# Kernel tuning notes

Hardware: AMD Instinct MI355X
Metric: run time of the kernel (lower is better)

The kernel has to match this reference:

```python
import jax, jax.numpy as jnp
import numpy as np

# dims: batch, encoder frames, encoder dim, pred-net hidden, joint dim, vocab (blank = V)
B, T, ENC, H, J, V = 32, 64, 1024, 320, 320, 1024
BLANK = V
MAXSYM = 2            # max_symbols_per_step
S = T * MAXSYM        # upper bound on loop-labels iterations (<= MAXSYM steps per frame due to force-blank)


def setup_inputs() -> dict:
    key = jax.random.key(0)
    ks = jax.random.split(key, 10)
    s = 0.05
    return {
        "x": jax.random.normal(ks[0], (B, T, ENC), jnp.float32),
        "out_len": jax.random.randint(ks[1], (B,), T // 2, T + 1, dtype=jnp.int32),
        "W_enc": jax.random.normal(ks[2], (ENC, J), jnp.float32) * s,
        "b_enc": jnp.zeros((J,), jnp.float32),
        "Emb": jax.random.normal(ks[3], (V, H), jnp.float32) * s,
        "W_ih": jax.random.normal(ks[4], (H, 4 * H), jnp.float32) * s,
        "W_hh": jax.random.normal(ks[5], (H, 4 * H), jnp.float32) * s,
        "b_lstm": jnp.zeros((4 * H,), jnp.float32),
        "W_pred": jax.random.normal(ks[6], (H, J), jnp.float32) * s,
        "b_pred": jnp.zeros((J,), jnp.float32),
        "W_out": jax.random.normal(ks[7], (J, V + 1), jnp.float32) * s,
        "b_out": jnp.zeros((V + 1,), jnp.float32),
    }


def _lstm_step(emb, h, c, W_ih, W_hh, b):
    g = emb @ W_ih + h @ W_hh + b
    i, f, gg, o = jnp.split(g, 4, axis=-1)
    c2 = jax.nn.sigmoid(f) * c + jax.nn.sigmoid(i) * jnp.tanh(gg)
    h2 = jax.nn.sigmoid(o) * jnp.tanh(c2)
    return h2, c2


def reference(x, out_len, W_enc, b_enc, Emb, W_ih, W_hh, b_lstm, W_pred, b_pred, W_out, b_out):
    # project_encoder once (as in the torch module)
    x_proj = x @ W_enc + b_enc                      # [B, T, J]
    # SOS step: zero embedding, zero LSTM state (decoder.predict(None, None))
    z = jnp.zeros((B, H), x.dtype)
    h0, c0 = _lstm_step(z, z, z, W_ih, W_hh, b_lstm)
    dec0 = h0 @ W_pred + b_pred                     # project_prednet

    def step(carry, _):
        time, symbols, h, c, dec = carry
        enc_t = jnp.take_along_axis(x_proj, time[:, None, None].astype(jnp.int32), axis=1)[:, 0]  # [B, J]
        logits = jax.nn.relu(enc_t + dec) @ W_out + b_out  # joint_after_projection, [B, V+1]
        scores = logits.max(-1)
        labels = jnp.argmax(logits, -1)
        active = time < out_len
        emit = active & (labels != BLANK)
        # prediction-network step for elements that emitted a non-blank label
        emb = Emb[jnp.where(emit, labels, 0)]
        h2, c2 = _lstm_step(emb, h, c, W_ih, W_hh, b_lstm)
        dec2 = h2 @ W_pred + b_pred
        m = emit[:, None]
        h = jnp.where(m, h2, h)
        c = jnp.where(m, c2, c)
        dec = jnp.where(m, dec2, dec)
        sym2 = jnp.where(emit, symbols + 1, jnp.zeros_like(symbols))
        force = emit & (sym2 >= MAXSYM)             # force blank after max_symbols on one frame
        advance = (active & ~emit) | force          # blank (or forced blank) advances time
        time2 = time + advance.astype(time.dtype)
        sym2 = jnp.where(advance, jnp.zeros_like(sym2), sym2)
        out = (jnp.where(emit, labels, BLANK).astype(jnp.int32),
               jnp.where(active, scores, jnp.zeros_like(scores)),
               time.astype(jnp.int32),
               emit)
        return (time2, sym2, h, c, dec), out

    init = (jnp.zeros((B,), jnp.int32), jnp.zeros((B,), jnp.int32), h0, c0, dec0)
    _, (lab, sc, tm, em) = jax.lax.scan(step, init, None, length=S)
    lengths = em.astype(jnp.int32).sum(0)
    # lab/sc/tm: [S, B] alignment-style records (BLANK filler when nothing emitted);
    # lengths: number of emitted (non-blank) labels per utterance -> equals batched_hyps contents.
    return lab, sc, tm, lengths
```

## Files before the change

### kernel.cpp

```cpp
#include <hip/hip_runtime.h>
#include <math.h>

typedef unsigned long long ull;

constexpr int Bn = 32, Tn = 64, Hn = 320, Jn = 320, Vn = 1024, Sn = 128;
constexpr int G4n = 1280, VP1 = 1025, WO4S = 1028;

constexpr int OFF_XP  = 0;
constexpr int OFF_G   = OFF_XP + Bn*Tn*Jn;
constexpr int OFF_WO4 = OFF_G + Vn*G4n;
constexpr int OFF_WH4 = OFF_WO4 + 80*WO4S*4;
constexpr int OFF_WP4 = OFF_WH4 + 80*G4n*4;
constexpr int OFF_CB  = OFF_WP4 + 80*Jn*4;
constexpr int OFF_DEC = OFF_CB + 2*Bn*Hn;
constexpr int OFF_GB  = OFF_DEC + 2*Bn*Jn;
constexpr int OFF_KEY = OFF_GB + 2*Bn*G4n;
constexpr int OFF_REC = OFF_KEY + 2*Bn*40*2;

__device__ __forceinline__ float sigmf(float x) { return 1.0f / (1.0f + expf(-x)); }

__device__ __forceinline__ ull pack_key(float v, int idx) {
    unsigned u = __float_as_uint(v);
    u = (u & 0x80000000u) ? ~u : (u | 0x80000000u);
    return ((ull)u << 32) | (unsigned)(0x7FFFFFFF - idx);
}
__device__ __forceinline__ float key_val(ull k) {
    unsigned u = (unsigned)(k >> 32);
    return __uint_as_float((u & 0x80000000u) ? (u & 0x7FFFFFFFu) : ~u);
}
__device__ __forceinline__ int key_idx(ull k) { return 0x7FFFFFFF - (int)(k & 0xFFFFFFFFu); }

__global__ __launch_bounds__(256) void gemm_bias(const float* __restrict__ A,
                                                 const float* __restrict__ Bm,
                                                 const float* __restrict__ bias,
                                                 float* __restrict__ C,
                                                 int M, int N, int K) {
    __shared__ float As[16][65];
    __shared__ float Bs[16][65];
    const int tx = threadIdx.x & 15, ty = threadIdx.x >> 4;
    const int n0 = blockIdx.x * 64, m0 = blockIdx.y * 64;
    float acc[4][4] = {};
    for (int k0 = 0; k0 < K; k0 += 16) {
        for (int i = threadIdx.x; i < 1024; i += 256) {
            int mm = i >> 4, kk = i & 15;
            As[kk][mm] = A[(m0 + mm) * K + k0 + kk];
            int kk2 = i >> 6, nn = i & 63;
            Bs[kk2][nn] = Bm[(k0 + kk2) * N + n0 + nn];
        }
        __syncthreads();
#pragma unroll
        for (int kk = 0; kk < 16; ++kk) {
            float av[4], bv[4];
#pragma unroll
            for (int r = 0; r < 4; ++r) { av[r] = As[kk][ty * 4 + r]; bv[r] = Bs[kk][tx * 4 + r]; }
#pragma unroll
            for (int i2 = 0; i2 < 4; ++i2)
#pragma unroll
                for (int j2 = 0; j2 < 4; ++j2) acc[i2][j2] += av[i2] * bv[j2];
        }
        __syncthreads();
    }
#pragma unroll
    for (int i2 = 0; i2 < 4; ++i2)
#pragma unroll
        for (int j2 = 0; j2 < 4; ++j2)
            C[(m0 + ty * 4 + i2) * N + n0 + tx * 4 + j2] = acc[i2][j2] + bias[n0 + tx * 4 + j2];
}

__global__ __launch_bounds__(256) void repack_wout4(const float* __restrict__ W,
                                                    float* __restrict__ W4) {
    const int k4 = blockIdx.x;
    for (int c = threadIdx.x; c < VP1; c += 256) {
        float4 v;
        v.x = W[(k4 * 4 + 0) * VP1 + c];
        v.y = W[(k4 * 4 + 1) * VP1 + c];
        v.z = W[(k4 * 4 + 2) * VP1 + c];
        v.w = W[(k4 * 4 + 3) * VP1 + c];
        ((float4*)W4)[(size_t)k4 * WO4S + c] = v;
    }
}
__global__ __launch_bounds__(256) void repack_whh4(const float* __restrict__ W,
                                                   float* __restrict__ W4) {
    const int k4 = blockIdx.x;
    for (int c = threadIdx.x; c < G4n; c += 256) {
        float4 v;
        v.x = W[(k4 * 4 + 0) * G4n + c];
        v.y = W[(k4 * 4 + 1) * G4n + c];
        v.z = W[(k4 * 4 + 2) * G4n + c];
        v.w = W[(k4 * 4 + 3) * G4n + c];
        ((float4*)W4)[(size_t)k4 * G4n + c] = v;
    }
}
__global__ __launch_bounds__(256) void repack_wpred4(const float* __restrict__ W,
                                                     float* __restrict__ W4) {
    const int k4 = blockIdx.x;
    for (int c = threadIdx.x; c < Jn; c += 256) {
        float4 v;
        v.x = W[(k4 * 4 + 0) * Jn + c];
        v.y = W[(k4 * 4 + 1) * Jn + c];
        v.z = W[(k4 * 4 + 2) * Jn + c];
        v.w = W[(k4 * 4 + 3) * Jn + c];
        ((float4*)W4)[(size_t)k4 * Jn + c] = v;
    }
}

__global__ __launch_bounds__(256, 1) void rnnt_step(
    const float* __restrict__ xp, const float* __restrict__ Gm,
    const float* __restrict__ Wo4, const float* __restrict__ Wh4,
    const float* __restrict__ Wp4,
    const float* __restrict__ b_out, const float* __restrict__ b_lstm,
    const float* __restrict__ b_pred, const int* __restrict__ out_len,
    float* __restrict__ cb, float* __restrict__ db, float* __restrict__ gb,
    ull* __restrict__ keys, int* __restrict__ rec, float* __restrict__ out,
    int L) {
    __shared__ __align__(16) float h_s[Hn];
    __shared__ __align__(16) float dec_s[Jn];
    __shared__ __align__(16) float f_s[Jn];
    __shared__ ull bk_s;

    const int w = blockIdx.x, tid = threadIdx.x;
    const int b = w & 31, m = w >> 5;
    const int ol = out_len[b];
    const float4* Wo4f = (const float4*)Wo4;
    const float4* Wh4f = (const float4*)Wh4;
    const float4* Wp4f = (const float4*)Wp4;
    const float4* h4 = (const float4*)h_s;
    const float4* f4 = (const float4*)f_s;

    int tnew, genN;
    bool doDec;
    if (L == 0) {
        for (int r = tid; r < Hn; r += 256) {
            float c0 = sigmf(b_lstm[r]) * tanhf(b_lstm[2 * Hn + r]);
            float h0 = sigmf(b_lstm[3 * Hn + r]) * tanhf(c0);
            h_s[r] = h0;
            int lc = r - m * 40;
            if (lc >= 0 && lc < 40) cb[b * Hn + r] = c0;
        }
        if (m == 0 && tid == 0) {
            int* rn = rec + b * 4;
            rn[0] = 0; rn[1] = 0; rn[2] = 0;
        }
        __syncthreads();
        tnew = 0; genN = 0; doDec = true;
    } else {
        const int* rp = rec + ((L - 1) & 1) * Bn * 4 + b * 4;
        const int told = rp[0], sold = rp[1], len = rp[2];
        if (tid < 64) {
            ull k = 0;
            if (tid < 33) k = keys[((L - 1) & 1) * Bn * 40 + b * 40 + tid];
#pragma unroll
            for (int d = 1; d < 64; d <<= 1) {
                ull o = __shfl_xor(k, d, 64);
                if (o > k) k = o;
            }
            if (tid == 0) bk_s = k;
        }
        __syncthreads();
        const ull bk = bk_s;
        const int label = key_idx(bk);
        const bool active = told < ol;
        const bool emit = active && (label != Vn);
        int sym2 = emit ? sold + 1 : 0;
        const bool force = emit && (sym2 >= 2);
        const bool advance = (active && !emit) || force;
        tnew = told + (advance ? 1 : 0);
        sym2 = advance ? 0 : sym2;
        const int newlen = len + (emit ? 1 : 0);
        if (m == 0 && tid == 0) {
            out[(L - 1) * Bn + b] = emit ? (float)label : 1024.0f;
            out[Sn * Bn + (L - 1) * Bn + b] = active ? key_val(bk) : 0.0f;
            out[2 * Sn * Bn + (L - 1) * Bn + b] = (float)told;
            int* rn = rec + (L & 1) * Bn * 4 + b * 4;
            rn[0] = tnew; rn[1] = sym2; rn[2] = newlen;
            if (L == Sn) out[3 * Sn * Bn + b] = (float)newlen;
        }
        if (L == Sn) return;
        if (tnew >= ol) return;
        genN = newlen;
        doDec = emit;
        if (emit) {
            const float* cv = cb + (len & 1) * Bn * Hn + b * Hn;
            float* cn = cb + (newlen & 1) * Bn * Hn + b * Hn;
            const float* gg = gb + (len & 1) * Bn * G4n + b * G4n;
            const float* gE = Gm + (size_t)label * G4n;
            {
                const int r = tid;
                float xi = gg[r] + gE[r];
                float xf = gg[Hn + r] + gE[Hn + r];
                float xg = gg[2 * Hn + r] + gE[2 * Hn + r];
                float xo = gg[3 * Hn + r] + gE[3 * Hn + r];
                float c2 = sigmf(xf) * cv[r] + sigmf(xi) * tanhf(xg);
                float h2 = sigmf(xo) * tanhf(c2);
                h_s[r] = h2;
                int lc = r - m * 40;
                if (lc >= 0 && lc < 40) cn[r] = c2;
            }
            if (tid < 64) {
                const int r = 256 + tid;
                float xi = gg[r] + gE[r];
                float xf = gg[Hn + r] + gE[Hn + r];
                float xg = gg[2 * Hn + r] + gE[2 * Hn + r];
                float xo = gg[3 * Hn + r] + gE[3 * Hn + r];
                float c2 = sigmf(xf) * cv[r] + sigmf(xi) * tanhf(xg);
                float h2 = sigmf(xo) * tanhf(c2);
                h_s[r] = h2;
                int lc = r - m * 40;
                if (lc >= 0 && lc < 40) cn[r] = c2;
            }
            __syncthreads();
        } else {
            dec_s[tid] = db[(len & 1) * Bn * Jn + b * Jn + tid];
            if (tid < 64) dec_s[256 + tid] = db[(len & 1) * Bn * Jn + b * Jn + 256 + tid];
        }
    }
    if (doDec) {
        float* dn = db + (genN & 1) * Bn * Jn + b * Jn;
        {
            const int c = tid;
            float ax = 0.f, ay = 0.f, az = 0.f, aw = 0.f;
#pragma unroll 20
            for (int k4 = 0; k4 < 80; ++k4) {
                float4 wv = Wp4f[(size_t)k4 * Jn + c];
                float4 hv = h4[k4];
                ax += wv.x * hv.x; ay += wv.y * hv.y;
                az += wv.z * hv.z; aw += wv.w * hv.w;
            }
            float d = b_pred[c] + ax + ay + az + aw;
            dec_s[c] = d;
            int lc = c - m * 40;
            if (lc >= 0 && lc < 40) dn[c] = d;
        }
        if (tid < 64) {
            const int c = 256 + tid;
            float ax = 0.f, ay = 0.f, az = 0.f, aw = 0.f;
#pragma unroll 20
            for (int k4 = 0; k4 < 80; ++k4) {
                float4 wv = Wp4f[(size_t)k4 * Jn + c];
                float4 hv = h4[k4];
                ax += wv.x * hv.x; ay += wv.y * hv.y;
                az += wv.z * hv.z; aw += wv.w * hv.w;
            }
            float d = b_pred[c] + ax + ay + az + aw;
            dec_s[c] = d;
            int lc = c - m * 40;
            if (lc >= 0 && lc < 40) dn[c] = d;
        }
        if (tid < 160) {
            const int c = m * 160 + tid;
            float ax = 0.f, ay = 0.f, az = 0.f, aw = 0.f;
#pragma unroll 20
            for (int k4 = 0; k4 < 80; ++k4) {
                float4 wv = Wh4f[(size_t)k4 * G4n + c];
                float4 hv = h4[k4];
                ax += wv.x * hv.x; ay += wv.y * hv.y;
                az += wv.z * hv.z; aw += wv.w * hv.w;
            }
            gb[(genN & 1) * Bn * G4n + b * G4n + c] = ax + ay + az + aw;
        }
    }
    {
        const int tc = tnew < (Tn - 1) ? tnew : (Tn - 1);
        const float* xr = xp + (size_t)(b * Tn + tc) * Jn;
        f_s[tid] = fmaxf(xr[tid] + dec_s[tid], 0.0f);
        if (tid < 64) f_s[256 + tid] = fmaxf(xr[256 + tid] + dec_s[256 + tid], 0.0f);
    }
    __syncthreads();
    {
        const int cl = tid >> 1, kh = tid & 1;
        const int c = m * 128 + cl;
        float ax = 0.f, ay = 0.f, az = 0.f, aw = 0.f;
#pragma unroll 10
        for (int k4 = kh * 40; k4 < kh * 40 + 40; ++k4) {
            float4 wv = Wo4f[(size_t)k4 * WO4S + c];
            float4 fv = f4[k4];
            ax += wv.x * fv.x; ay += wv.y * fv.y;
            az += wv.z * fv.z; aw += wv.w * fv.w;
        }
        float part = ax + ay + az + aw;
        part += __shfl_xor(part, 1, 64);
        ull key = pack_key(part + b_out[c], c);
#pragma unroll
        for (int d = 1; d < 64; d <<= 1) {
            ull o = __shfl_xor(key, d, 64);
            if (o > key) key = o;
        }
        if ((tid & 63) == 0) keys[(L & 1) * Bn * 40 + b * 40 + m * 4 + (tid >> 6)] = key;
    }
    if (m == 7 && tid >= 192) {
        const int l = tid - 192;
        float4 wv = Wo4f[(size_t)l * WO4S + Vn];
        float4 fv = f4[l];
        float p = wv.x * fv.x + wv.y * fv.y + wv.z * fv.z + wv.w * fv.w;
        if (l < 16) {
            float4 wv2 = Wo4f[(size_t)(64 + l) * WO4S + Vn];
            float4 fv2 = f4[64 + l];
            p += wv2.x * fv2.x + wv2.y * fv2.y + wv2.z * fv2.z + wv2.w * fv2.w;
        }
#pragma unroll
        for (int d = 1; d < 64; d <<= 1) p += __shfl_xor(p, d, 64);
        if (l == 0) keys[(L & 1) * Bn * 40 + b * 40 + 32] = pack_key(p + b_out[Vn], Vn);
    }
}

extern "C" void kernel_launch(void* const* d_in, const int* in_sizes, int n_in,
                              void* d_out, int out_size, void* d_ws, size_t ws_size,
                              hipStream_t stream) {
    (void)in_sizes; (void)n_in; (void)out_size; (void)ws_size;
    const float* x      = (const float*)d_in[0];
    const int*   outlen = (const int*)d_in[1];
    const float* W_enc  = (const float*)d_in[2];
    const float* b_enc  = (const float*)d_in[3];
    const float* Emb    = (const float*)d_in[4];
    const float* W_ih   = (const float*)d_in[5];
    const float* W_hh   = (const float*)d_in[6];
    const float* b_lstm = (const float*)d_in[7];
    const float* W_pred = (const float*)d_in[8];
    const float* b_pred = (const float*)d_in[9];
    const float* W_out  = (const float*)d_in[10];
    const float* b_out  = (const float*)d_in[11];

    float* ws  = (float*)d_ws;
    float* xp  = ws + OFF_XP;
    float* Gm  = ws + OFF_G;
    float* Wo4 = ws + OFF_WO4;
    float* Wh4 = ws + OFF_WH4;
    float* Wp4 = ws + OFF_WP4;
    float* cb  = ws + OFF_CB;
    float* db  = ws + OFF_DEC;
    float* gb  = ws + OFF_GB;
    ull*   keys = (ull*)(ws + OFF_KEY);
    int*   rec  = (int*)(ws + OFF_REC);

    gemm_bias<<<dim3(5, 32), 256, 0, stream>>>(x, W_enc, b_enc, xp, Bn * Tn, Jn, 1024);
    gemm_bias<<<dim3(20, 16), 256, 0, stream>>>(Emb, W_ih, b_lstm, Gm, Vn, G4n, Hn);
    repack_wout4<<<80, 256, 0, stream>>>(W_out, Wo4);
    repack_whh4<<<80, 256, 0, stream>>>(W_hh, Wh4);
    repack_wpred4<<<80, 256, 0, stream>>>(W_pred, Wp4);

    for (int L = 0; L <= Sn; ++L)
        rnnt_step<<<256, 256, 0, stream>>>(xp, Gm, Wo4, Wh4, Wp4,
                                           b_out, b_lstm, b_pred, outlen,
                                           cb, db, gb, keys, rec,
                                           (float*)d_out, L);
}
```

Before: 2.100 ms.

## Merge preamble kernels and widen step blocks to one thread per hidden unit

```diff
diff --git a/kernel.cpp b/kernel.cpp
--- a/kernel.cpp
+++ b/kernel.cpp
@@ -30,15 +30,14 @@
 }
 __device__ __forceinline__ int key_idx(ull k) { return 0x7FFFFFFF - (int)(k & 0xFFFFFFFFu); }
 
-__global__ __launch_bounds__(256) void gemm_bias(const float* __restrict__ A,
-                                                 const float* __restrict__ Bm,
-                                                 const float* __restrict__ bias,
-                                                 float* __restrict__ C,
-                                                 int M, int N, int K) {
-    __shared__ float As[16][65];
-    __shared__ float Bs[16][65];
+__device__ __forceinline__ void gemm_tile(const float* __restrict__ A,
+                                          const float* __restrict__ Bm,
+                                          const float* __restrict__ bias,
+                                          float* __restrict__ C,
+                                          int M, int N, int K, int bx, int by,
+                                          float (*As)[65], float (*Bs)[65]) {
     const int tx = threadIdx.x & 15, ty = threadIdx.x >> 4;
-    const int n0 = blockIdx.x * 64, m0 = blockIdx.y * 64;
+    const int n0 = bx * 64, m0 = by * 64;
     float acc[4][4] = {};
     for (int k0 = 0; k0 < K; k0 += 16) {
         for (int i = threadIdx.x; i < 1024; i += 256) {
@@ -67,44 +66,56 @@
             C[(m0 + ty * 4 + i2) * N + n0 + tx * 4 + j2] = acc[i2][j2] + bias[n0 + tx * 4 + j2];
 }
 
-__global__ __launch_bounds__(256) void repack_wout4(const float* __restrict__ W,
-                                                    float* __restrict__ W4) {
-    const int k4 = blockIdx.x;
-    for (int c = threadIdx.x; c < VP1; c += 256) {
-        float4 v;
-        v.x = W[(k4 * 4 + 0) * VP1 + c];
-        v.y = W[(k4 * 4 + 1) * VP1 + c];
-        v.z = W[(k4 * 4 + 2) * VP1 + c];
-        v.w = W[(k4 * 4 + 3) * VP1 + c];
-        ((float4*)W4)[(size_t)k4 * WO4S + c] = v;
-    }
-}
-__global__ __launch_bounds__(256) void repack_whh4(const float* __restrict__ W,
-                                                   float* __restrict__ W4) {
-    const int k4 = blockIdx.x;
-    for (int c = threadIdx.x; c < G4n; c += 256) {
-        float4 v;
-        v.x = W[(k4 * 4 + 0) * G4n + c];
-        v.y = W[(k4 * 4 + 1) * G4n + c];
-        v.z = W[(k4 * 4 + 2) * G4n + c];
-        v.w = W[(k4 * 4 + 3) * G4n + c];
-        ((float4*)W4)[(size_t)k4 * G4n + c] = v;
-    }
-}
-__global__ __launch_bounds__(256) void repack_wpred4(const float* __restrict__ W,
-                                                     float* __restrict__ W4) {
-    const int k4 = blockIdx.x;
-    for (int c = threadIdx.x; c < Jn; c += 256) {
-        float4 v;
-        v.x = W[(k4 * 4 + 0) * Jn + c];
-        v.y = W[(k4 * 4 + 1) * Jn + c];
-        v.z = W[(k4 * 4 + 2) * Jn + c];
-        v.w = W[(k4 * 4 + 3) * Jn + c];
-        ((float4*)W4)[(size_t)k4 * Jn + c] = v;
-    }
-}
-
-__global__ __launch_bounds__(256, 1) void rnnt_step(
+__global__ __launch_bounds__(256) void preamble(
+    const float* __restrict__ x, const float* __restrict__ W_enc,
+    const float* __restrict__ b_enc, const float* __restrict__ Emb,
+    const float* __restrict__ W_ih, const float* __restrict__ b_lstm,
+    const float* __restrict__ W_hh, const float* __restrict__ W_pred,
+    const float* __restrict__ W_out,
+    float* __restrict__ xp, float* __restrict__ Gm,
+    float* __restrict__ Wo4, float* __restrict__ Wh4, float* __restrict__ Wp4) {
+    __shared__ float As[16][65];
+    __shared__ float Bs[16][65];
+    const int blk = blockIdx.x;
+    if (blk < 160) {
+        gemm_tile(x, W_enc, b_enc, xp, Bn * Tn, Jn, 1024, blk % 5, blk / 5, As, Bs);
+    } else if (blk < 480) {
+        const int t = blk - 160;
+        gemm_tile(Emb, W_ih, b_lstm, Gm, Vn, G4n, Hn, t % 20, t / 20, As, Bs);
+    } else if (blk < 560) {
+        const int k4 = blk - 480;
+        for (int c = threadIdx.x; c < VP1; c += 256) {
+            float4 v;
+            v.x = W_out[(k4 * 4 + 0) * VP1 + c];
+            v.y = W_out[(k4 * 4 + 1) * VP1 + c];
+            v.z = W_out[(k4 * 4 + 2) * VP1 + c];
+            v.w = W_out[(k4 * 4 + 3) * VP1 + c];
+            ((float4*)Wo4)[(size_t)k4 * WO4S + c] = v;
+        }
+    } else if (blk < 640) {
+        const int k4 = blk - 560;
+        for (int c = threadIdx.x; c < G4n; c += 256) {
+            float4 v;
+            v.x = W_hh[(k4 * 4 + 0) * G4n + c];
+            v.y = W_hh[(k4 * 4 + 1) * G4n + c];
+            v.z = W_hh[(k4 * 4 + 2) * G4n + c];
+            v.w = W_hh[(k4 * 4 + 3) * G4n + c];
+            ((float4*)Wh4)[(size_t)k4 * G4n + c] = v;
+        }
+    } else {
+        const int k4 = blk - 640;
+        for (int c = threadIdx.x; c < Jn; c += 256) {
+            float4 v;
+            v.x = W_pred[(k4 * 4 + 0) * Jn + c];
+            v.y = W_pred[(k4 * 4 + 1) * Jn + c];
+            v.z = W_pred[(k4 * 4 + 2) * Jn + c];
+            v.w = W_pred[(k4 * 4 + 3) * Jn + c];
+            ((float4*)Wp4)[(size_t)k4 * Jn + c] = v;
+        }
+    }
+}
+
+__global__ __launch_bounds__(320, 1) void rnnt_step(
     const float* __restrict__ xp, const float* __restrict__ Gm,
     const float* __restrict__ Wo4, const float* __restrict__ Wh4,
     const float* __restrict__ Wp4,
@@ -130,7 +141,8 @@
     int tnew, genN;
     bool doDec;
     if (L == 0) {
-        for (int r = tid; r < Hn; r += 256) {
+        {
+            const int r = tid;
             float c0 = sigmf(b_lstm[r]) * tanhf(b_lstm[2 * Hn + r]);
             float h0 = sigmf(b_lstm[3 * Hn + r]) * tanhf(c0);
             h_s[r] = h0;
@@ -146,6 +158,11 @@
     } else {
         const int* rp = rec + ((L - 1) & 1) * Bn * 4 + b * 4;
         const int told = rp[0], sold = rp[1], len = rp[2];
+        const float* gq = gb + (size_t)((len & 1) * Bn + b) * G4n;
+        const float* cv = cb + (size_t)((len & 1) * Bn + b) * Hn;
+        float g0 = gq[tid], g1 = gq[Hn + tid], g2 = gq[2 * Hn + tid], g3 = gq[3 * Hn + tid];
+        float crv = cv[tid];
+        asm volatile("" ::: "memory");
         if (tid < 64) {
             ull k = 0;
             if (tid < 33) k = keys[((L - 1) & 1) * Bn * 40 + b * 40 + tid];
@@ -180,42 +197,24 @@
         genN = newlen;
         doDec = emit;
         if (emit) {
-            const float* cv = cb + (len & 1) * Bn * Hn + b * Hn;
-            float* cn = cb + (newlen & 1) * Bn * Hn + b * Hn;
-            const float* gg = gb + (len & 1) * Bn * G4n + b * G4n;
             const float* gE = Gm + (size_t)label * G4n;
-            {
-                const int r = tid;
-                float xi = gg[r] + gE[r];
-                float xf = gg[Hn + r] + gE[Hn + r];
-                float xg = gg[2 * Hn + r] + gE[2 * Hn + r];
-                float xo = gg[3 * Hn + r] + gE[3 * Hn + r];
-                float c2 = sigmf(xf) * cv[r] + sigmf(xi) * tanhf(xg);
-                float h2 = sigmf(xo) * tanhf(c2);
-                h_s[r] = h2;
-                int lc = r - m * 40;
-                if (lc >= 0 && lc < 40) cn[r] = c2;
-            }
-            if (tid < 64) {
-                const int r = 256 + tid;
-                float xi = gg[r] + gE[r];
-                float xf = gg[Hn + r] + gE[Hn + r];
-                float xg = gg[2 * Hn + r] + gE[2 * Hn + r];
-                float xo = gg[3 * Hn + r] + gE[3 * Hn + r];
-                float c2 = sigmf(xf) * cv[r] + sigmf(xi) * tanhf(xg);
-                float h2 = sigmf(xo) * tanhf(c2);
-                h_s[r] = h2;
-                int lc = r - m * 40;
-                if (lc >= 0 && lc < 40) cn[r] = c2;
-            }
-            __syncthreads();
+            float xi = g0 + gE[tid];
+            float xf = g1 + gE[Hn + tid];
+            float xg = g2 + gE[2 * Hn + tid];
+            float xo = g3 + gE[3 * Hn + tid];
+            float c2 = sigmf(xf) * crv + sigmf(xi) * tanhf(xg);
+            float h2 = sigmf(xo) * tanhf(c2);
+            h_s[tid] = h2;
+            int lc = tid - m * 40;
+            if (lc >= 0 && lc < 40)
+                cb[(size_t)((newlen & 1) * Bn + b) * Hn + tid] = c2;
         } else {
-            dec_s[tid] = db[(len & 1) * Bn * Jn + b * Jn + tid];
-            if (tid < 64) dec_s[256 + tid] = db[(len & 1) * Bn * Jn + b * Jn + 256 + tid];
-        }
+            dec_s[tid] = db[(size_t)((len & 1) * Bn + b) * Jn + tid];
+        }
+        __syncthreads();
     }
     if (doDec) {
-        float* dn = db + (genN & 1) * Bn * Jn + b * Jn;
+        float* dn = db + (size_t)((genN & 1) * Bn + b) * Jn;
         {
             const int c = tid;
             float ax = 0.f, ay = 0.f, az = 0.f, aw = 0.f;
@@ -231,21 +230,6 @@
             int lc = c - m * 40;
             if (lc >= 0 && lc < 40) dn[c] = d;
         }
-        if (tid < 64) {
-            const int c = 256 + tid;
-            float ax = 0.f, ay = 0.f, az = 0.f, aw = 0.f;
-#pragma unroll 20
-            for (int k4 = 0; k4 < 80; ++k4) {
-                float4 wv = Wp4f[(size_t)k4 * Jn + c];
-                float4 hv = h4[k4];
-                ax += wv.x * hv.x; ay += wv.y * hv.y;
-                az += wv.z * hv.z; aw += wv.w * hv.w;
-            }
-            float d = b_pred[c] + ax + ay + az + aw;
-            dec_s[c] = d;
-            int lc = c - m * 40;
-            if (lc >= 0 && lc < 40) dn[c] = d;
-        }
         if (tid < 160) {
             const int c = m * 160 + tid;
             float ax = 0.f, ay = 0.f, az = 0.f, aw = 0.f;
@@ -256,17 +240,17 @@
                 ax += wv.x * hv.x; ay += wv.y * hv.y;
                 az += wv.z * hv.z; aw += wv.w * hv.w;
             }
-            gb[(genN & 1) * Bn * G4n + b * G4n + c] = ax + ay + az + aw;
-        }
-    }
+            gb[(size_t)((genN & 1) * Bn + b) * G4n + c] = ax + ay + az + aw;
+        }
+    }
+    __syncthreads();
     {
         const int tc = tnew < (Tn - 1) ? tnew : (Tn - 1);
         const float* xr = xp + (size_t)(b * Tn + tc) * Jn;
         f_s[tid] = fmaxf(xr[tid] + dec_s[tid], 0.0f);
-        if (tid < 64) f_s[256 + tid] = fmaxf(xr[256 + tid] + dec_s[256 + tid], 0.0f);
     }
     __syncthreads();
-    {
+    if (tid < 256) {
         const int cl = tid >> 1, kh = tid & 1;
         const int c = m * 128 + cl;
         float ax = 0.f, ay = 0.f, az = 0.f, aw = 0.f;
@@ -285,10 +269,10 @@
             ull o = __shfl_xor(key, d, 64);
             if (o > key) key = o;
         }
-        if ((tid & 63) == 0) keys[(L & 1) * Bn * 40 + b * 40 + m * 4 + (tid >> 6)] = key;
-    }
-    if (m == 7 && tid >= 192) {
-        const int l = tid - 192;
+        if ((tid & 63) == 0)
+            keys[(L & 1) * Bn * 40 + b * 40 + m * 4 + (tid >> 6)] = key;
+    } else if (m == 7) {
+        const int l = tid - 256;
         float4 wv = Wo4f[(size_t)l * WO4S + Vn];
         float4 fv = f4[l];
         float p = wv.x * fv.x + wv.y * fv.y + wv.z * fv.z + wv.w * fv.w;
@@ -332,14 +316,12 @@
     ull*   keys = (ull*)(ws + OFF_KEY);
     int*   rec  = (int*)(ws + OFF_REC);
 
-    gemm_bias<<<dim3(5, 32), 256, 0, stream>>>(x, W_enc, b_enc, xp, Bn * Tn, Jn, 1024);
-    gemm_bias<<<dim3(20, 16), 256, 0, stream>>>(Emb, W_ih, b_lstm, Gm, Vn, G4n, Hn);
-    repack_wout4<<<80, 256, 0, stream>>>(W_out, Wo4);
-    repack_whh4<<<80, 256, 0, stream>>>(W_hh, Wh4);
-    repack_wpred4<<<80, 256, 0, stream>>>(W_pred, Wp4);
+    preamble<<<720, 256, 0, stream>>>(x, W_enc, b_enc, Emb, W_ih, b_lstm,
+                                      W_hh, W_pred, W_out,
+                                      xp, Gm, Wo4, Wh4, Wp4);
 
     for (int L = 0; L <= Sn; ++L)
-        rnnt_step<<<256, 256, 0, stream>>>(xp, Gm, Wo4, Wh4, Wp4,
+        rnnt_step<<<256, 320, 0, stream>>>(xp, Gm, Wo4, Wh4, Wp4,
                                            b_out, b_lstm, b_pred, outlen,
                                            cb, db, gb, keys, rec,
                                            (float*)d_out, L);
```

Result: faster. 2.036 ms (-3.1%).
